# Kernel tuning notes

Measured on AMD Instinct MI355X. Metric: run time of the kernel, lower is better.

Reference implementation:

```python
import jax, jax.numpy as jnp
import numpy as np

N = 4_194_304   # samples per polarization
L = 513         # impulse response taps


def setup_inputs() -> dict:
    key = jax.random.key(0)
    k1, k2, k3, k4 = jax.random.split(key, 4)
    tx_real = jax.random.normal(k1, (2, N), dtype=jnp.float32)
    tx_imag = jax.random.normal(k2, (2, N), dtype=jnp.float32)
    h_real = jax.random.normal(k3, (L,), dtype=jnp.float32)
    h_imag = jax.random.normal(k4, (L,), dtype=jnp.float32)
    return {"tx_real": tx_real, "tx_imag": tx_imag, "h_real": h_real, "h_imag": h_imag}


def reference(tx_real, tx_imag, h_real, h_imag):
    # Dual-pol complex baseband signal [2, N]; same taps h [L] applied to each pol.
    tx = tx_real + 1j * tx_imag          # complex64 [2, N]
    h = h_real + 1j * h_imag             # complex64 [L]
    n_out = tx.shape[-1] + h.shape[0] - 1  # 'full' convolution length
    # FFT-based full convolution, both polarizations batched in one FFT call
    # (mathematically identical to overlap-save convolution in 'full' mode).
    X = jnp.fft.fft(tx, n=n_out, axis=-1)   # [2, n_out]
    H = jnp.fft.fft(h, n=n_out)             # [n_out]
    y = jnp.fft.ifft(X * H[None, :], axis=-1)  # [2, n_out] complex
    # Return real/imag stacked so the output is a real array: [2, n_out, 2]
    return jnp.stack([y.real, y.imag], axis=-1)
```

## Files before the change

### kernel.cpp

```cpp
#include <hip/hip_runtime.h>
#include <hip/hip_bf16.h>


#define NSAMP 4194304
#define LTAPS 513
#define NOUT  (NSAMP + LTAPS - 1)

#define BLK       512
#define WAVE_OUT  1024
#define BLOCK_OUT 8192
#define HALO      512
#define XELEMS    (BLOCK_OUT + HALO + 16)
#define NB        34
#define HROWS     592
#define GRID      256
#define NT        513
#define XEL_MINI  1552
#define SITER     5

typedef __attribute__((ext_vector_type(8)))  short short8;
typedef __attribute__((ext_vector_type(4)))  short short4v;
typedef __attribute__((ext_vector_type(4)))  int   int4v;
typedef __attribute__((ext_vector_type(16))) float float16v;

__device__ __forceinline__ int xswz(int e) { return e ^ (((e >> 6) & 7) << 3); }
#define XSZ XELEMS

__device__ __forceinline__ short f2b(float f) {
    __bf16 b = (__bf16)f;
    return __builtin_bit_cast(short, b);
}

__global__ __launch_bounds__(BLK)
void build_h(const float* __restrict__ hr, const float* __restrict__ hi,
             short* __restrict__ hh) {
    int R = blockIdx.x * BLK + threadIdx.x;
    if (R < HROWS) {
        short8 vr, vi;
        #pragma unroll
        for (int j = 0; j < 8; ++j) {
            int idx = R - 24 - j;
            bool ok = (idx >= 0) && (idx < LTAPS);
            vr[j] = f2b(ok ? hr[idx] : 0.0f);
            vi[j] = f2b(ok ? hi[idx] : 0.0f);
        }
        *(short8*)(hh + (size_t)(0 * HROWS + R) * 8) = vr;
        *(short8*)(hh + (size_t)(1 * HROWS + R) * 8) = vi;
    }
}

#define MFMA32(A, B, C) __builtin_amdgcn_mfma_f32_32x32x16_bf16((A), (B), (C), 0, 0, 0)

__device__ __forceinline__ short8 bneg8(short8 v) {
    int4v t = __builtin_bit_cast(int4v, v);
    t ^= (int4v){(int)0x80008000, (int)0x80008000, (int)0x80008000, (int)0x80008000};
    return __builtin_bit_cast(short8, t);
}

__device__ __forceinline__ bool tile_edge(int t) { return (t == 0) || (t >= 511); }

__global__ __launch_bounds__(BLK, 2)
void fir_pipe(const float* __restrict__ txr_all, const float* __restrict__ txi_all,
              const short* __restrict__ hh, float2* __restrict__ out) {
    const int bid = blockIdx.x;
    const int tid = threadIdx.x;

    __shared__ __align__(16) short xs[2][4][XSZ];
    __shared__ __align__(16) short hl[2 * HROWS * 8];

    {
        const int4* src = (const int4*)hh;
        int4* dst = (int4*)hl;
        #pragma unroll
        for (int it = 0; it < 3; ++it) {
            int idx = tid + it * BLK;
            if (idx < 2 * HROWS) dst[idx] = src[idx];
        }
    }

    float4 fr[2][SITER], fi[2][SITER];

    auto stage_load = [&](int t) {
        if (tile_edge(t)) return;
        const int N0 = t * BLOCK_OUT;
        #pragma unroll
        for (int p = 0; p < 2; ++p) {
            const float* __restrict__ xr_g = txr_all + (size_t)p * NSAMP + (N0 - HALO);
            const float* __restrict__ xi_g = txi_all + (size_t)p * NSAMP + (N0 - HALO);
            #pragma unroll
            for (int it = 0; it < SITER; ++it) {
                int e = (tid + it * BLK) * 4;
                if (e < XELEMS) {
                    fr[p][it] = *(const float4*)(xr_g + e);
                    fi[p][it] = *(const float4*)(xi_g + e);
                }
            }
        }
    };

    auto stage_write = [&](int t, int buf) {
        if (!tile_edge(t)) {
            #pragma unroll
            for (int p = 0; p < 2; ++p) {
                #pragma unroll
                for (int it = 0; it < SITER; ++it) {
                    int e = (tid + it * BLK) * 4;
                    if (e < XELEMS) {
                        int ls = xswz(e);
                        float4 r = fr[p][it], i = fi[p][it];
                        short4v vr = { f2b(r.x), f2b(r.y), f2b(r.z), f2b(r.w) };
                        short4v vi = { f2b(i.x), f2b(i.y), f2b(i.z), f2b(i.w) };
                        *(short4v*)(&xs[buf][2 * p + 0][ls]) = vr;
                        *(short4v*)(&xs[buf][2 * p + 1][ls]) = vi;
                    }
                }
            }
        } else {
            const int N0  = t * BLOCK_OUT;
            const int xel = (t == NT - 1) ? XEL_MINI : XELEMS;
            for (int p = 0; p < 2; ++p) {
                const float* __restrict__ xr_g = txr_all + (size_t)p * NSAMP;
                const float* __restrict__ xi_g = txi_all + (size_t)p * NSAMP;
                for (int it = 0; it < SITER; ++it) {
                    int e = (tid + it * BLK) * 4;
                    if (e < xel) {
                        int g = N0 - HALO + e;
                        float r0, r1, r2, r3, i0, i1, i2, i3;
                        if (g >= 0 && g + 3 < NSAMP) {
                            float4 frv = *(const float4*)(xr_g + g);
                            float4 fiv = *(const float4*)(xi_g + g);
                            r0 = frv.x; r1 = frv.y; r2 = frv.z; r3 = frv.w;
                            i0 = fiv.x; i1 = fiv.y; i2 = fiv.z; i3 = fiv.w;
                        } else {
                            int gc0 = min(max(g + 0, 0), NSAMP - 1);
                            int gc1 = min(max(g + 1, 0), NSAMP - 1);
                            int gc2 = min(max(g + 2, 0), NSAMP - 1);
                            int gc3 = min(max(g + 3, 0), NSAMP - 1);
                            r0 = (g + 0 >= 0 && g + 0 < NSAMP) ? xr_g[gc0] : 0.0f;
                            r1 = (g + 1 >= 0 && g + 1 < NSAMP) ? xr_g[gc1] : 0.0f;
                            r2 = (g + 2 >= 0 && g + 2 < NSAMP) ? xr_g[gc2] : 0.0f;
                            r3 = (g + 3 >= 0 && g + 3 < NSAMP) ? xr_g[gc3] : 0.0f;
                            i0 = (g + 0 >= 0 && g + 0 < NSAMP) ? xi_g[gc0] : 0.0f;
                            i1 = (g + 1 >= 0 && g + 1 < NSAMP) ? xi_g[gc1] : 0.0f;
                            i2 = (g + 2 >= 0 && g + 2 < NSAMP) ? xi_g[gc2] : 0.0f;
                            i3 = (g + 3 >= 0 && g + 3 < NSAMP) ? xi_g[gc3] : 0.0f;
                        }
                        int ls = xswz(e);
                        short4v vr = { f2b(r0), f2b(r1), f2b(r2), f2b(r3) };
                        short4v vi = { f2b(i0), f2b(i1), f2b(i2), f2b(i3) };
                        *(short4v*)(&xs[buf][2 * p + 0][ls]) = vr;
                        *(short4v*)(&xs[buf][2 * p + 1][ls]) = vi;
                    }
                }
            }
        }
    };

    const int lane = tid & 63;
    const int wave = tid >> 6;
    const int cc   = lane & 31;
    const int half = lane >> 5;
    const short* hp0 = hl + (size_t)(cc - 8 * half + 8) * 8;

    auto compute_store = [&](int t, int buf) {
        const int N0 = t * BLOCK_OUT;
        const int nw = N0 + wave * WAVE_OUT;
        if (nw >= NOUT) return;

        float16v zero = {0.f,0.f,0.f,0.f,0.f,0.f,0.f,0.f,0.f,0.f,0.f,0.f,0.f,0.f,0.f,0.f};
        float16v acc_re0 = zero, acc_im0 = zero, acc_re1 = zero, acc_im1 = zero;

        const int    ebase = HALO + wave * WAVE_OUT + 32 * cc + 8 * half + 16;
        const short* xb    = &xs[buf][0][0];

        int ls0 = xswz(ebase);
        short8 fxr0 = *(const short8*)(xb + ls0);
        short8 fxi0 = *(const short8*)(xb + XSZ + ls0);
        short8 fxr1 = *(const short8*)(xb + 2 * XSZ + ls0);
        short8 fxi1 = *(const short8*)(xb + 3 * XSZ + ls0);
        short8 fhr  = *(const short8*)(hp0);
        short8 fhi  = *(const short8*)(hp0 + (size_t)HROWS * 8);

        #pragma unroll 2
        for (int b = 0; b < NB; ++b) {
            int en = ebase - 16 * (b + 1);
            en = en < 0 ? 0 : en;
            int lsn = xswz(en);
            short8 nxr0 = *(const short8*)(xb + lsn);
            short8 nxi0 = *(const short8*)(xb + XSZ + lsn);
            short8 nxr1 = *(const short8*)(xb + 2 * XSZ + lsn);
            short8 nxi1 = *(const short8*)(xb + 3 * XSZ + lsn);
            const short* hn = hp0 + (size_t)(16 * (b + 1)) * 8;
            short8 nhr = *(const short8*)(hn);
            short8 nhi = *(const short8*)(hn + (size_t)HROWS * 8);

            short8 fnhi = bneg8(fhi);
            acc_re0 = MFMA32(fxr0, fhr,  acc_re0);
            acc_im0 = MFMA32(fxi0, fhr,  acc_im0);
            acc_re1 = MFMA32(fxr1, fhr,  acc_re1);
            acc_im1 = MFMA32(fxi1, fhr,  acc_im1);
            acc_re0 = MFMA32(fxi0, fnhi, acc_re0);
            acc_im0 = MFMA32(fxr0, fhi,  acc_im0);
            acc_re1 = MFMA32(fxi1, fnhi, acc_re1);
            acc_im1 = MFMA32(fxr1, fhi,  acc_im1);

            fxr0 = nxr0; fxi0 = nxi0; fxr1 = nxr1; fxi1 = nxi1;
            fhr  = nhr;  fhi  = nhi;
        }

        float2* __restrict__ op0 = out;
        float2* __restrict__ op1 = out + (size_t)NOUT;
        #pragma unroll
        for (int v = 0; v < 16; ++v) {
            int row = (v & 3) + 8 * (v >> 2) + 4 * half;
            int n = nw + 32 * row + cc;
            if (n < NOUT) {
                op0[n] = make_float2(acc_re0[v], acc_im0[v]);
                op1[n] = make_float2(acc_re1[v], acc_im1[v]);
            }
        }
    };

    stage_load(bid);
    stage_write(bid, 0);
    __syncthreads();

    int cur = 0;
    for (int t = bid; t < NT; t += GRID) {
        int tn = t + GRID;
        if (tn < NT) stage_load(tn);
        compute_store(t, cur);
        if (tn < NT) {
            stage_write(tn, cur ^ 1);
            __syncthreads();
        }
        cur ^= 1;
    }
}

extern "C" void kernel_launch(void* const* d_in, const int* in_sizes, int n_in,
                              void* d_out, int out_size, void* d_ws, size_t ws_size,
                              hipStream_t stream) {
    const float* txr = (const float*)d_in[0];
    const float* txi = (const float*)d_in[1];
    const float* hr  = (const float*)d_in[2];
    const float* hi  = (const float*)d_in[3];
    float2* out = (float2*)d_out;
    short* hh = (short*)d_ws;

    build_h<<<dim3((HROWS + BLK - 1) / BLK), BLK, 0, stream>>>(hr, hi, hh);

    fir_pipe<<<dim3(GRID), BLK, 0, stream>>>(txr, txi, hh, out);
}
```

Before: 141.8 us.

## Interleave next-tile global loads and LDS writes into the MFMA loop

The next tile's global float4 loads and bf16 conversion with LDS writes are spread across the even iterations of a now fully unrolled MFMA tap loop, instead of being done in bulk around the compute. The output stores move after the barrier, and the edge-tile staging is merged into a single general stage function. The register prefetch of the next MFMA operands is dropped in favour of direct loads per iteration. This aims to hide global load latency behind matrix work, at the cost of more live registers (20 float4 staging buffers plus accumulators) and a larger unrolled code body.

```diff
diff --git a/kernel.cpp b/kernel.cpp
--- a/kernel.cpp
+++ b/kernel.cpp
@@ -15,7 +15,6 @@
 #define HROWS     592
 #define GRID      256
 #define NT        513
-#define XEL_MINI  1552
 #define SITER     5
 
 typedef __attribute__((ext_vector_type(8)))  short short8;
@@ -78,79 +77,41 @@
         }
     }
 
-    float4 fr[2][SITER], fi[2][SITER];
-
-    auto stage_load = [&](int t) {
-        if (tile_edge(t)) return;
+    auto stage_tile = [&](int t, int buf) {
         const int N0 = t * BLOCK_OUT;
-        #pragma unroll
+        short* xnb = &xs[buf][0][0];
         for (int p = 0; p < 2; ++p) {
-            const float* __restrict__ xr_g = txr_all + (size_t)p * NSAMP + (N0 - HALO);
-            const float* __restrict__ xi_g = txi_all + (size_t)p * NSAMP + (N0 - HALO);
-            #pragma unroll
+            const float* __restrict__ xr_g = txr_all + (size_t)p * NSAMP;
+            const float* __restrict__ xi_g = txi_all + (size_t)p * NSAMP;
             for (int it = 0; it < SITER; ++it) {
                 int e = (tid + it * BLK) * 4;
                 if (e < XELEMS) {
-                    fr[p][it] = *(const float4*)(xr_g + e);
-                    fi[p][it] = *(const float4*)(xi_g + e);
-                }
-            }
-        }
-    };
-
-    auto stage_write = [&](int t, int buf) {
-        if (!tile_edge(t)) {
-            #pragma unroll
-            for (int p = 0; p < 2; ++p) {
-                #pragma unroll
-                for (int it = 0; it < SITER; ++it) {
-                    int e = (tid + it * BLK) * 4;
-                    if (e < XELEMS) {
-                        int ls = xswz(e);
-                        float4 r = fr[p][it], i = fi[p][it];
-                        short4v vr = { f2b(r.x), f2b(r.y), f2b(r.z), f2b(r.w) };
-                        short4v vi = { f2b(i.x), f2b(i.y), f2b(i.z), f2b(i.w) };
-                        *(short4v*)(&xs[buf][2 * p + 0][ls]) = vr;
-                        *(short4v*)(&xs[buf][2 * p + 1][ls]) = vi;
+                    int g = N0 - HALO + e;
+                    float r0, r1, r2, r3, i0, i1, i2, i3;
+                    if (g >= 0 && g + 3 < NSAMP) {
+                        float4 frv = *(const float4*)(xr_g + g);
+                        float4 fiv = *(const float4*)(xi_g + g);
+                        r0 = frv.x; r1 = frv.y; r2 = frv.z; r3 = frv.w;
+                        i0 = fiv.x; i1 = fiv.y; i2 = fiv.z; i3 = fiv.w;
+                    } else {
+                        int gc0 = min(max(g + 0, 0), NSAMP - 1);
+                        int gc1 = min(max(g + 1, 0), NSAMP - 1);
+                        int gc2 = min(max(g + 2, 0), NSAMP - 1);
+                        int gc3 = min(max(g + 3, 0), NSAMP - 1);
+                        r0 = (g + 0 >= 0 && g + 0 < NSAMP) ? xr_g[gc0] : 0.0f;
+                        r1 = (g + 1 >= 0 && g + 1 < NSAMP) ? xr_g[gc1] : 0.0f;
+                        r2 = (g + 2 >= 0 && g + 2 < NSAMP) ? xr_g[gc2] : 0.0f;
+                        r3 = (g + 3 >= 0 && g + 3 < NSAMP) ? xr_g[gc3] : 0.0f;
+                        i0 = (g + 0 >= 0 && g + 0 < NSAMP) ? xi_g[gc0] : 0.0f;
+                        i1 = (g + 1 >= 0 && g + 1 < NSAMP) ? xi_g[gc1] : 0.0f;
+                        i2 = (g + 2 >= 0 && g + 2 < NSAMP) ? xi_g[gc2] : 0.0f;
+                        i3 = (g + 3 >= 0 && g + 3 < NSAMP) ? xi_g[gc3] : 0.0f;
                     }
-                }
-            }
-        } else {
-            const int N0  = t * BLOCK_OUT;
-            const int xel = (t == NT - 1) ? XEL_MINI : XELEMS;
-            for (int p = 0; p < 2; ++p) {
-                const float* __restrict__ xr_g = txr_all + (size_t)p * NSAMP;
-                const float* __restrict__ xi_g = txi_all + (size_t)p * NSAMP;
-                for (int it = 0; it < SITER; ++it) {
-                    int e = (tid + it * BLK) * 4;
-                    if (e < xel) {
-                        int g = N0 - HALO + e;
-                        float r0, r1, r2, r3, i0, i1, i2, i3;
-                        if (g >= 0 && g + 3 < NSAMP) {
-                            float4 frv = *(const float4*)(xr_g + g);
-                            float4 fiv = *(const float4*)(xi_g + g);
-                            r0 = frv.x; r1 = frv.y; r2 = frv.z; r3 = frv.w;
-                            i0 = fiv.x; i1 = fiv.y; i2 = fiv.z; i3 = fiv.w;
-                        } else {
-                            int gc0 = min(max(g + 0, 0), NSAMP - 1);
-                            int gc1 = min(max(g + 1, 0), NSAMP - 1);
-                            int gc2 = min(max(g + 2, 0), NSAMP - 1);
-                            int gc3 = min(max(g + 3, 0), NSAMP - 1);
-                            r0 = (g + 0 >= 0 && g + 0 < NSAMP) ? xr_g[gc0] : 0.0f;
-                            r1 = (g + 1 >= 0 && g + 1 < NSAMP) ? xr_g[gc1] : 0.0f;
-                            r2 = (g + 2 >= 0 && g + 2 < NSAMP) ? xr_g[gc2] : 0.0f;
-                            r3 = (g + 3 >= 0 && g + 3 < NSAMP) ? xr_g[gc3] : 0.0f;
-                            i0 = (g + 0 >= 0 && g + 0 < NSAMP) ? xi_g[gc0] : 0.0f;
-                            i1 = (g + 1 >= 0 && g + 1 < NSAMP) ? xi_g[gc1] : 0.0f;
-                            i2 = (g + 2 >= 0 && g + 2 < NSAMP) ? xi_g[gc2] : 0.0f;
-                            i3 = (g + 3 >= 0 && g + 3 < NSAMP) ? xi_g[gc3] : 0.0f;
-                        }
-                        int ls = xswz(e);
-                        short4v vr = { f2b(r0), f2b(r1), f2b(r2), f2b(r3) };
-                        short4v vi = { f2b(i0), f2b(i1), f2b(i2), f2b(i3) };
-                        *(short4v*)(&xs[buf][2 * p + 0][ls]) = vr;
-                        *(short4v*)(&xs[buf][2 * p + 1][ls]) = vi;
-                    }
+                    int ls = xswz(e);
+                    short4v vr = { f2b(r0), f2b(r1), f2b(r2), f2b(r3) };
+                    short4v vi = { f2b(i0), f2b(i1), f2b(i2), f2b(i3) };
+                    *(short4v*)(xnb + (size_t)(2 * p + 0) * XSZ + ls) = vr;
+                    *(short4v*)(xnb + (size_t)(2 * p + 1) * XSZ + ls) = vi;
                 }
             }
         }
@@ -160,79 +121,103 @@
     const int wave = tid >> 6;
     const int cc   = lane & 31;
     const int half = lane >> 5;
-    const short* hp0 = hl + (size_t)(cc - 8 * half + 8) * 8;
-
-    auto compute_store = [&](int t, int buf) {
-        const int N0 = t * BLOCK_OUT;
-        const int nw = N0 + wave * WAVE_OUT;
-        if (nw >= NOUT) return;
+    const short* hp0  = hl + (size_t)(cc - 8 * half + 8) * 8;
+    const int   ebase = HALO + wave * WAVE_OUT + 32 * cc + 8 * half + 16;
+
+    stage_tile(bid, 0);
+    asm volatile("s_waitcnt lgkmcnt(0)" ::: "memory");
+    __builtin_amdgcn_s_barrier();
+    __builtin_amdgcn_sched_barrier(0);
+
+    int cur = 0;
+    for (int t = bid; t < NT; t += GRID) {
+        const int  tn = t + GRID;
+        const bool do_stage = (tn < NT) && !tile_edge(tn);
+        const int  N0 = t * BLOCK_OUT;
+        const int  nw = N0 + wave * WAVE_OUT;
+        const bool did = (nw < NOUT);
 
         float16v zero = {0.f,0.f,0.f,0.f,0.f,0.f,0.f,0.f,0.f,0.f,0.f,0.f,0.f,0.f,0.f,0.f};
         float16v acc_re0 = zero, acc_im0 = zero, acc_re1 = zero, acc_im1 = zero;
 
-        const int    ebase = HALO + wave * WAVE_OUT + 32 * cc + 8 * half + 16;
-        const short* xb    = &xs[buf][0][0];
-
-        int ls0 = xswz(ebase);
-        short8 fxr0 = *(const short8*)(xb + ls0);
-        short8 fxi0 = *(const short8*)(xb + XSZ + ls0);
-        short8 fxr1 = *(const short8*)(xb + 2 * XSZ + ls0);
-        short8 fxi1 = *(const short8*)(xb + 3 * XSZ + ls0);
-        short8 fhr  = *(const short8*)(hp0);
-        short8 fhi  = *(const short8*)(hp0 + (size_t)HROWS * 8);
-
-        #pragma unroll 2
-        for (int b = 0; b < NB; ++b) {
-            int en = ebase - 16 * (b + 1);
-            en = en < 0 ? 0 : en;
-            int lsn = xswz(en);
-            short8 nxr0 = *(const short8*)(xb + lsn);
-            short8 nxi0 = *(const short8*)(xb + XSZ + lsn);
-            short8 nxr1 = *(const short8*)(xb + 2 * XSZ + lsn);
-            short8 nxi1 = *(const short8*)(xb + 3 * XSZ + lsn);
-            const short* hn = hp0 + (size_t)(16 * (b + 1)) * 8;
-            short8 nhr = *(const short8*)(hn);
-            short8 nhi = *(const short8*)(hn + (size_t)HROWS * 8);
-
-            short8 fnhi = bneg8(fhi);
-            acc_re0 = MFMA32(fxr0, fhr,  acc_re0);
-            acc_im0 = MFMA32(fxi0, fhr,  acc_im0);
-            acc_re1 = MFMA32(fxr1, fhr,  acc_re1);
-            acc_im1 = MFMA32(fxi1, fhr,  acc_im1);
-            acc_re0 = MFMA32(fxi0, fnhi, acc_re0);
-            acc_im0 = MFMA32(fxr0, fhi,  acc_im0);
-            acc_re1 = MFMA32(fxi1, fnhi, acc_re1);
-            acc_im1 = MFMA32(fxr1, fhi,  acc_im1);
-
-            fxr0 = nxr0; fxi0 = nxi0; fxr1 = nxr1; fxi1 = nxi1;
-            fhr  = nhr;  fhi  = nhi;
-        }
-
-        float2* __restrict__ op0 = out;
-        float2* __restrict__ op1 = out + (size_t)NOUT;
-        #pragma unroll
-        for (int v = 0; v < 16; ++v) {
-            int row = (v & 3) + 8 * (v >> 2) + 4 * half;
-            int n = nw + 32 * row + cc;
-            if (n < NOUT) {
-                op0[n] = make_float2(acc_re0[v], acc_im0[v]);
-                op1[n] = make_float2(acc_re1[v], acc_im1[v]);
+        if (did) {
+            const short* xb  = &xs[cur][0][0];
+            short*       xnb = &xs[cur ^ 1][0][0];
+            const int    sg  = tn * BLOCK_OUT - HALO;
+            float4 sr[10], si[10];
+
+            #pragma unroll
+            for (int b = 0; b < NB; ++b) {
+                if ((b & 1) == 0 && b < 20) {
+                    if (do_stage) {
+                        const int j  = b >> 1;
+                        const int p  = (j >= SITER) ? 1 : 0;
+                        const int it = j - p * SITER;
+                        const int e  = (tid + it * BLK) * 4;
+                        if (e < XELEMS) {
+                            const float* xr_g = txr_all + (size_t)p * NSAMP + sg + e;
+                            const float* xi_g = txi_all + (size_t)p * NSAMP + sg + e;
+                            sr[j] = *(const float4*)xr_g;
+                            si[j] = *(const float4*)xi_g;
+                        }
+                    }
+                }
+                if ((b & 1) == 0 && b >= 8 && b < 28) {
+                    if (do_stage) {
+                        const int j  = (b - 8) >> 1;
+                        const int p  = (j >= SITER) ? 1 : 0;
+                        const int it = j - p * SITER;
+                        const int e  = (tid + it * BLK) * 4;
+                        if (e < XELEMS) {
+                            int ls = xswz(e);
+                            float4 r = sr[j], i = si[j];
+                            short4v vr = { f2b(r.x), f2b(r.y), f2b(r.z), f2b(r.w) };
+                            short4v vi = { f2b(i.x), f2b(i.y), f2b(i.z), f2b(i.w) };
+                            *(short4v*)(xnb + (size_t)(2 * p + 0) * XSZ + ls) = vr;
+                            *(short4v*)(xnb + (size_t)(2 * p + 1) * XSZ + ls) = vi;
+                        }
+                    }
+                }
+
+                int ls = xswz(ebase - 16 * b);
+                short8 fxr0 = *(const short8*)(xb + ls);
+                short8 fxi0 = *(const short8*)(xb + XSZ + ls);
+                short8 fxr1 = *(const short8*)(xb + 2 * XSZ + ls);
+                short8 fxi1 = *(const short8*)(xb + 3 * XSZ + ls);
+                const short* hp = hp0 + (size_t)(16 * b) * 8;
+                short8 fhr = *(const short8*)(hp);
+                short8 fhi = *(const short8*)(hp + (size_t)HROWS * 8);
+
+                short8 fnhi = bneg8(fhi);
+                acc_re0 = MFMA32(fxr0, fhr,  acc_re0);
+                acc_im0 = MFMA32(fxi0, fhr,  acc_im0);
+                acc_re1 = MFMA32(fxr1, fhr,  acc_re1);
+                acc_im1 = MFMA32(fxi1, fhr,  acc_im1);
+                acc_re0 = MFMA32(fxi0, fnhi, acc_re0);
+                acc_im0 = MFMA32(fxr0, fhi,  acc_im0);
+                acc_re1 = MFMA32(fxi1, fnhi, acc_re1);
+                acc_im1 = MFMA32(fxr1, fhi,  acc_im1);
             }
         }
-    };
-
-    stage_load(bid);
-    stage_write(bid, 0);
-    __syncthreads();
-
-    int cur = 0;
-    for (int t = bid; t < NT; t += GRID) {
-        int tn = t + GRID;
-        if (tn < NT) stage_load(tn);
-        compute_store(t, cur);
-        if (tn < NT) {
-            stage_write(tn, cur ^ 1);
-            __syncthreads();
+
+        if (tn < NT && tile_edge(tn)) stage_tile(tn, cur ^ 1);
+
+        asm volatile("s_waitcnt lgkmcnt(0)" ::: "memory");
+        __builtin_amdgcn_s_barrier();
+        __builtin_amdgcn_sched_barrier(0);
+
+        if (did) {
+            float2* __restrict__ op0 = out;
+            float2* __restrict__ op1 = out + (size_t)NOUT;
+            #pragma unroll
+            for (int v = 0; v < 16; ++v) {
+                int row = (v & 3) + 8 * (v >> 2) + 4 * half;
+                int n = nw + 32 * row + cc;
+                if (n < NOUT) {
+                    op0[n] = make_float2(acc_re0[v], acc_im0[v]);
+                    op1[n] = make_float2(acc_re1[v], acc_im1[v]);
+                }
+            }
         }
         cur ^= 1;
     }
```

Result: no change. 139.3 us (-1.7%).

## Halve block and tile size, pad LDS layout, restructure prefetch/compute/store pipeline

Applied to the files above, without the earlier changes.

Shrinks each block to 256 threads and each tile to 4096 outputs, so each of the 256 blocks now handles about four tiles instead of two. The XOR swizzle is replaced by a padded LDS layout. The loop is reordered so that global prefetch, MFMA compute, the LDS write of the next tile and the output stores run in a fixed sequence, with clamped unconditional loads on interior tiles and explicit scheduling barriers. The aim is to overlap loads with MFMA work and to cut edge-handling branches. In exchange, each CU now holds fewer waves, which weakens latency hiding for the MFMA and LDS work.

```diff
diff --git a/kernel.cpp b/kernel.cpp
--- a/kernel.cpp
+++ b/kernel.cpp
@@ -6,16 +6,16 @@
 #define LTAPS 513
 #define NOUT  (NSAMP + LTAPS - 1)
 
-#define BLK       512
+#define BLK       256
 #define WAVE_OUT  1024
-#define BLOCK_OUT 8192
+#define BLOCK_OUT 4096
 #define HALO      512
 #define XELEMS    (BLOCK_OUT + HALO + 16)
+#define EMAX      (XELEMS - 4)
 #define NB        34
 #define HROWS     592
 #define GRID      256
-#define NT        513
-#define XEL_MINI  1552
+#define NT        ((NOUT + BLOCK_OUT - 1) / BLOCK_OUT)
 #define SITER     5
 
 typedef __attribute__((ext_vector_type(8)))  short short8;
@@ -23,8 +23,8 @@
 typedef __attribute__((ext_vector_type(4)))  int   int4v;
 typedef __attribute__((ext_vector_type(16))) float float16v;
 
-__device__ __forceinline__ int xswz(int e) { return e ^ (((e >> 6) & 7) << 3); }
-#define XSZ XELEMS
+__device__ __forceinline__ int xswz(int e) { return e + ((e >> 5) << 3); }
+#define XSZ 5776
 
 __device__ __forceinline__ short f2b(float f) {
     __bf16 b = (__bf16)f;
@@ -57,9 +57,9 @@
     return __builtin_bit_cast(short8, t);
 }
 
-__device__ __forceinline__ bool tile_edge(int t) { return (t == 0) || (t >= 511); }
-
-__global__ __launch_bounds__(BLK, 2)
+__device__ __forceinline__ bool tile_edge(int t) { return (t == 0) || (t >= 1023); }
+
+__global__ __launch_bounds__(BLK, 1)
 void fir_pipe(const float* __restrict__ txr_all, const float* __restrict__ txi_all,
               const short* __restrict__ hh, float2* __restrict__ out) {
     const int bid = blockIdx.x;
@@ -72,85 +72,48 @@
         const int4* src = (const int4*)hh;
         int4* dst = (int4*)hl;
         #pragma unroll
-        for (int it = 0; it < 3; ++it) {
+        for (int it = 0; it < 5; ++it) {
             int idx = tid + it * BLK;
-            if (idx < 2 * HROWS) dst[idx] = src[idx];
+            if (idx < 2 * HROWS / 2 * 2 * 8 / 8) {}
+            if (idx < (2 * HROWS * 8) / 8) dst[idx] = src[idx];
         }
     }
 
-    float4 fr[2][SITER], fi[2][SITER];
-
-    auto stage_load = [&](int t) {
-        if (tile_edge(t)) return;
+    auto stage_slow = [&](int t, int buf) {
         const int N0 = t * BLOCK_OUT;
         #pragma unroll
         for (int p = 0; p < 2; ++p) {
-            const float* __restrict__ xr_g = txr_all + (size_t)p * NSAMP + (N0 - HALO);
-            const float* __restrict__ xi_g = txi_all + (size_t)p * NSAMP + (N0 - HALO);
-            #pragma unroll
+            const float* __restrict__ xr_g = txr_all + (size_t)p * NSAMP;
+            const float* __restrict__ xi_g = txi_all + (size_t)p * NSAMP;
             for (int it = 0; it < SITER; ++it) {
                 int e = (tid + it * BLK) * 4;
                 if (e < XELEMS) {
-                    fr[p][it] = *(const float4*)(xr_g + e);
-                    fi[p][it] = *(const float4*)(xi_g + e);
-                }
-            }
-        }
-    };
-
-    auto stage_write = [&](int t, int buf) {
-        if (!tile_edge(t)) {
-            #pragma unroll
-            for (int p = 0; p < 2; ++p) {
-                #pragma unroll
-                for (int it = 0; it < SITER; ++it) {
-                    int e = (tid + it * BLK) * 4;
-                    if (e < XELEMS) {
-                        int ls = xswz(e);
-                        float4 r = fr[p][it], i = fi[p][it];
-                        short4v vr = { f2b(r.x), f2b(r.y), f2b(r.z), f2b(r.w) };
-                        short4v vi = { f2b(i.x), f2b(i.y), f2b(i.z), f2b(i.w) };
-                        *(short4v*)(&xs[buf][2 * p + 0][ls]) = vr;
-                        *(short4v*)(&xs[buf][2 * p + 1][ls]) = vi;
+                    int g = N0 - HALO + e;
+                    float r0, r1, r2, r3, i0, i1, i2, i3;
+                    if (g >= 0 && g + 3 < NSAMP) {
+                        float4 frv = *(const float4*)(xr_g + g);
+                        float4 fiv = *(const float4*)(xi_g + g);
+                        r0 = frv.x; r1 = frv.y; r2 = frv.z; r3 = frv.w;
+                        i0 = fiv.x; i1 = fiv.y; i2 = fiv.z; i3 = fiv.w;
+                    } else {
+                        int gc0 = min(max(g + 0, 0), NSAMP - 1);
+                        int gc1 = min(max(g + 1, 0), NSAMP - 1);
+                        int gc2 = min(max(g + 2, 0), NSAMP - 1);
+                        int gc3 = min(max(g + 3, 0), NSAMP - 1);
+                        r0 = (g + 0 >= 0 && g + 0 < NSAMP) ? xr_g[gc0] : 0.0f;
+                        r1 = (g + 1 >= 0 && g + 1 < NSAMP) ? xr_g[gc1] : 0.0f;
+                        r2 = (g + 2 >= 0 && g + 2 < NSAMP) ? xr_g[gc2] : 0.0f;
+                        r3 = (g + 3 >= 0 && g + 3 < NSAMP) ? xr_g[gc3] : 0.0f;
+                        i0 = (g + 0 >= 0 && g + 0 < NSAMP) ? xi_g[gc0] : 0.0f;
+                        i1 = (g + 1 >= 0 && g + 1 < NSAMP) ? xi_g[gc1] : 0.0f;
+                        i2 = (g + 2 >= 0 && g + 2 < NSAMP) ? xi_g[gc2] : 0.0f;
+                        i3 = (g + 3 >= 0 && g + 3 < NSAMP) ? xi_g[gc3] : 0.0f;
                     }
-                }
-            }
-        } else {
-            const int N0  = t * BLOCK_OUT;
-            const int xel = (t == NT - 1) ? XEL_MINI : XELEMS;
-            for (int p = 0; p < 2; ++p) {
-                const float* __restrict__ xr_g = txr_all + (size_t)p * NSAMP;
-                const float* __restrict__ xi_g = txi_all + (size_t)p * NSAMP;
-                for (int it = 0; it < SITER; ++it) {
-                    int e = (tid + it * BLK) * 4;
-                    if (e < xel) {
-                        int g = N0 - HALO + e;
-                        float r0, r1, r2, r3, i0, i1, i2, i3;
-                        if (g >= 0 && g + 3 < NSAMP) {
-                            float4 frv = *(const float4*)(xr_g + g);
-                            float4 fiv = *(const float4*)(xi_g + g);
-                            r0 = frv.x; r1 = frv.y; r2 = frv.z; r3 = frv.w;
-                            i0 = fiv.x; i1 = fiv.y; i2 = fiv.z; i3 = fiv.w;
-                        } else {
-                            int gc0 = min(max(g + 0, 0), NSAMP - 1);
-                            int gc1 = min(max(g + 1, 0), NSAMP - 1);
-                            int gc2 = min(max(g + 2, 0), NSAMP - 1);
-                            int gc3 = min(max(g + 3, 0), NSAMP - 1);
-                            r0 = (g + 0 >= 0 && g + 0 < NSAMP) ? xr_g[gc0] : 0.0f;
-                            r1 = (g + 1 >= 0 && g + 1 < NSAMP) ? xr_g[gc1] : 0.0f;
-                            r2 = (g + 2 >= 0 && g + 2 < NSAMP) ? xr_g[gc2] : 0.0f;
-                            r3 = (g + 3 >= 0 && g + 3 < NSAMP) ? xr_g[gc3] : 0.0f;
-                            i0 = (g + 0 >= 0 && g + 0 < NSAMP) ? xi_g[gc0] : 0.0f;
-                            i1 = (g + 1 >= 0 && g + 1 < NSAMP) ? xi_g[gc1] : 0.0f;
-                            i2 = (g + 2 >= 0 && g + 2 < NSAMP) ? xi_g[gc2] : 0.0f;
-                            i3 = (g + 3 >= 0 && g + 3 < NSAMP) ? xi_g[gc3] : 0.0f;
-                        }
-                        int ls = xswz(e);
-                        short4v vr = { f2b(r0), f2b(r1), f2b(r2), f2b(r3) };
-                        short4v vi = { f2b(i0), f2b(i1), f2b(i2), f2b(i3) };
-                        *(short4v*)(&xs[buf][2 * p + 0][ls]) = vr;
-                        *(short4v*)(&xs[buf][2 * p + 1][ls]) = vi;
-                    }
+                    int ls = xswz(e);
+                    short4v vr = { f2b(r0), f2b(r1), f2b(r2), f2b(r3) };
+                    short4v vi = { f2b(i0), f2b(i1), f2b(i2), f2b(i3) };
+                    *(short4v*)(&xs[buf][2 * p + 0][ls]) = vr;
+                    *(short4v*)(&xs[buf][2 * p + 1][ls]) = vi;
                 }
             }
         }
@@ -160,80 +123,114 @@
     const int wave = tid >> 6;
     const int cc   = lane & 31;
     const int half = lane >> 5;
-    const short* hp0 = hl + (size_t)(cc - 8 * half + 8) * 8;
-
-    auto compute_store = [&](int t, int buf) {
-        const int N0 = t * BLOCK_OUT;
-        const int nw = N0 + wave * WAVE_OUT;
-        if (nw >= NOUT) return;
+    const short* hp0  = hl + (size_t)(cc - 8 * half + 8) * 8;
+    const int   ebase = HALO + wave * WAVE_OUT + 32 * cc + 8 * half + 16;
+
+    stage_slow(bid, 0);
+    __syncthreads();
+
+    int cur = 0;
+    for (int t = bid; t < NT; t += GRID) {
+        const int  tn   = t + GRID;
+        const bool pipe = (tn < NT) && !tile_edge(tn);
+        const int  nw   = t * BLOCK_OUT + wave * WAVE_OUT;
+        const bool did  = (nw < NOUT);
+
+        float4 ld0[SITER], ld1[SITER], ld2[SITER], ld3[SITER];
+        if (pipe) {
+            const long gb  = (long)tn * BLOCK_OUT - HALO;
+            const float* g0 = txr_all + gb;
+            const float* g1 = txi_all + gb;
+            const float* g2 = txr_all + (size_t)NSAMP + gb;
+            const float* g3 = txi_all + (size_t)NSAMP + gb;
+            #pragma unroll
+            for (int it = 0; it < SITER; ++it) {
+                int e = min((tid + it * BLK) * 4, EMAX);
+                ld0[it] = *(const float4*)(g0 + e);
+                ld1[it] = *(const float4*)(g1 + e);
+                ld2[it] = *(const float4*)(g2 + e);
+                ld3[it] = *(const float4*)(g3 + e);
+            }
+        }
+        asm volatile("" ::: "memory");
+        __builtin_amdgcn_sched_barrier(0);
 
         float16v zero = {0.f,0.f,0.f,0.f,0.f,0.f,0.f,0.f,0.f,0.f,0.f,0.f,0.f,0.f,0.f,0.f};
         float16v acc_re0 = zero, acc_im0 = zero, acc_re1 = zero, acc_im1 = zero;
-
-        const int    ebase = HALO + wave * WAVE_OUT + 32 * cc + 8 * half + 16;
-        const short* xb    = &xs[buf][0][0];
-
-        int ls0 = xswz(ebase);
-        short8 fxr0 = *(const short8*)(xb + ls0);
-        short8 fxi0 = *(const short8*)(xb + XSZ + ls0);
-        short8 fxr1 = *(const short8*)(xb + 2 * XSZ + ls0);
-        short8 fxi1 = *(const short8*)(xb + 3 * XSZ + ls0);
-        short8 fhr  = *(const short8*)(hp0);
-        short8 fhi  = *(const short8*)(hp0 + (size_t)HROWS * 8);
-
-        #pragma unroll 2
-        for (int b = 0; b < NB; ++b) {
-            int en = ebase - 16 * (b + 1);
-            en = en < 0 ? 0 : en;
-            int lsn = xswz(en);
-            short8 nxr0 = *(const short8*)(xb + lsn);
-            short8 nxi0 = *(const short8*)(xb + XSZ + lsn);
-            short8 nxr1 = *(const short8*)(xb + 2 * XSZ + lsn);
-            short8 nxi1 = *(const short8*)(xb + 3 * XSZ + lsn);
-            const short* hn = hp0 + (size_t)(16 * (b + 1)) * 8;
-            short8 nhr = *(const short8*)(hn);
-            short8 nhi = *(const short8*)(hn + (size_t)HROWS * 8);
-
-            short8 fnhi = bneg8(fhi);
-            acc_re0 = MFMA32(fxr0, fhr,  acc_re0);
-            acc_im0 = MFMA32(fxi0, fhr,  acc_im0);
-            acc_re1 = MFMA32(fxr1, fhr,  acc_re1);
-            acc_im1 = MFMA32(fxi1, fhr,  acc_im1);
-            acc_re0 = MFMA32(fxi0, fnhi, acc_re0);
-            acc_im0 = MFMA32(fxr0, fhi,  acc_im0);
-            acc_re1 = MFMA32(fxi1, fnhi, acc_re1);
-            acc_im1 = MFMA32(fxr1, fhi,  acc_im1);
-
-            fxr0 = nxr0; fxi0 = nxi0; fxr1 = nxr1; fxi1 = nxi1;
-            fhr  = nhr;  fhi  = nhi;
-        }
-
-        float2* __restrict__ op0 = out;
-        float2* __restrict__ op1 = out + (size_t)NOUT;
-        #pragma unroll
-        for (int v = 0; v < 16; ++v) {
-            int row = (v & 3) + 8 * (v >> 2) + 4 * half;
-            int n = nw + 32 * row + cc;
-            if (n < NOUT) {
-                op0[n] = make_float2(acc_re0[v], acc_im0[v]);
-                op1[n] = make_float2(acc_re1[v], acc_im1[v]);
-            }
-        }
-    };
-
-    stage_load(bid);
-    stage_write(bid, 0);
-    __syncthreads();
-
-    int cur = 0;
-    for (int t = bid; t < NT; t += GRID) {
-        int tn = t + GRID;
-        if (tn < NT) stage_load(tn);
-        compute_store(t, cur);
-        if (tn < NT) {
-            stage_write(tn, cur ^ 1);
-            __syncthreads();
-        }
+        if (did) {
+            const short* xb = &xs[cur][0][0];
+            int ls0 = xswz(ebase);
+            short8 fxr0 = *(const short8*)(xb + ls0);
+            short8 fxi0 = *(const short8*)(xb + XSZ + ls0);
+            short8 fxr1 = *(const short8*)(xb + 2 * XSZ + ls0);
+            short8 fxi1 = *(const short8*)(xb + 3 * XSZ + ls0);
+            short8 fhr  = *(const short8*)(hp0);
+            short8 fhi  = *(const short8*)(hp0 + (size_t)HROWS * 8);
+
+            #pragma unroll 2
+            for (int b = 0; b < NB; ++b) {
+                int en = ebase - 16 * (b + 1);
+                en = en < 0 ? 0 : en;
+                int lsn = xswz(en);
+                short8 nxr0 = *(const short8*)(xb + lsn);
+                short8 nxi0 = *(const short8*)(xb + XSZ + lsn);
+                short8 nxr1 = *(const short8*)(xb + 2 * XSZ + lsn);
+                short8 nxi1 = *(const short8*)(xb + 3 * XSZ + lsn);
+                const short* hn = hp0 + (size_t)(16 * (b + 1)) * 8;
+                short8 nhr = *(const short8*)(hn);
+                short8 nhi = *(const short8*)(hn + (size_t)HROWS * 8);
+
+                short8 fnhi = bneg8(fhi);
+                acc_re0 = MFMA32(fxr0, fhr,  acc_re0);
+                acc_im0 = MFMA32(fxi0, fhr,  acc_im0);
+                acc_re1 = MFMA32(fxr1, fhr,  acc_re1);
+                acc_im1 = MFMA32(fxi1, fhr,  acc_im1);
+                acc_re0 = MFMA32(fxi0, fnhi, acc_re0);
+                acc_im0 = MFMA32(fxr0, fhi,  acc_im0);
+                acc_re1 = MFMA32(fxi1, fnhi, acc_re1);
+                acc_im1 = MFMA32(fxr1, fhi,  acc_im1);
+
+                fxr0 = nxr0; fxi0 = nxi0; fxr1 = nxr1; fxi1 = nxi1;
+                fhr  = nhr;  fhi  = nhi;
+            }
+        }
+
+        if (pipe) {
+            #pragma unroll
+            for (int it = 0; it < SITER; ++it) {
+                int e  = min((tid + it * BLK) * 4, EMAX);
+                int ls = xswz(e);
+                float4 v0 = ld0[it], v1 = ld1[it], v2 = ld2[it], v3 = ld3[it];
+                short4v s0 = { f2b(v0.x), f2b(v0.y), f2b(v0.z), f2b(v0.w) };
+                short4v s1 = { f2b(v1.x), f2b(v1.y), f2b(v1.z), f2b(v1.w) };
+                short4v s2 = { f2b(v2.x), f2b(v2.y), f2b(v2.z), f2b(v2.w) };
+                short4v s3 = { f2b(v3.x), f2b(v3.y), f2b(v3.z), f2b(v3.w) };
+                *(short4v*)(&xs[cur ^ 1][0][ls]) = s0;
+                *(short4v*)(&xs[cur ^ 1][1][ls]) = s1;
+                *(short4v*)(&xs[cur ^ 1][2][ls]) = s2;
+                *(short4v*)(&xs[cur ^ 1][3][ls]) = s3;
+            }
+        } else if (tn < NT) {
+            stage_slow(tn, cur ^ 1);
+        }
+
+        if (did) {
+            float2* __restrict__ op0 = out;
+            float2* __restrict__ op1 = out + (size_t)NOUT;
+            #pragma unroll
+            for (int v = 0; v < 16; ++v) {
+                int row = (v & 3) + 8 * (v >> 2) + 4 * half;
+                int n = nw + 32 * row + cc;
+                if (n < NOUT) {
+                    op0[n] = make_float2(acc_re0[v], acc_im0[v]);
+                    op1[n] = make_float2(acc_re1[v], acc_im1[v]);
+                }
+            }
+        }
+
+        asm volatile("s_waitcnt lgkmcnt(0)" ::: "memory");
+        __builtin_amdgcn_s_barrier();
+        __builtin_amdgcn_sched_barrier(0);
         cur ^= 1;
     }
 }
```

After: 149.6 us. +5.5%, slower.
